# Performance work log

Hardware: AMD Instinct MI355X
Metric: run time of the kernel (lower is better)

## Reference

```python
import jax, jax.numpy as jnp
import numpy as np

N_NODES = 100000
N_EDGES = 1000000
NODE_DIM = 64
HIDDEN_DIM = 128


def setup_inputs() -> dict:
    key = jax.random.key(0)
    ks = jax.random.split(key, 9)
    x = jax.random.normal(ks[0], (N_NODES, NODE_DIM), dtype=jnp.float32)
    y = jax.random.normal(ks[1], (N_NODES, NODE_DIM), dtype=jnp.float32)
    edge_index = jax.random.randint(ks[2], (2, N_EDGES), 0, N_NODES, dtype=jnp.int64)
    pos_x = jax.random.normal(ks[3], (N_NODES, 3), dtype=jnp.float32)
    pos_y = jax.random.normal(ks[4], (N_NODES, 3), dtype=jnp.float32)
    in_dim = NODE_DIM * 2 + 1
    # Kaiming-uniform-ish init like torch Linear
    lim1 = 1.0 / np.sqrt(in_dim)
    lim2 = 1.0 / np.sqrt(HIDDEN_DIM)
    W1 = jax.random.uniform(ks[5], (in_dim, HIDDEN_DIM), jnp.float32, -lim1, lim1)
    b1 = jax.random.uniform(ks[6], (HIDDEN_DIM,), jnp.float32, -lim1, lim1)
    W2 = jax.random.uniform(ks[7], (HIDDEN_DIM, 1), jnp.float32, -lim2, lim2)
    b2 = jax.random.uniform(ks[8], (1,), jnp.float32, -lim2, lim2)
    return {"x": x, "y": y, "edge_index": edge_index, "pos_x": pos_x,
            "pos_y": pos_y, "W1": W1, "b1": b1, "W2": W2, "b2": b2}


def reference(x, y, edge_index, pos_x, pos_y, W1, b1, W2, b2):
    src = edge_index[0]
    dst = edge_index[1]
    # per-edge euclidean distance between endpoint positions  [E]
    d = pos_x[src] - pos_y[dst]                      # [E, 3]
    dist = jnp.sqrt(jnp.sum(d * d, axis=1))          # [E]
    # gather + concat: [E, node_dim*2 + 1]
    mlp_in = jnp.concatenate([x[src], y[dst], dist[:, None]], axis=1)
    h = jax.nn.relu(mlp_in @ W1 + b1)                # [E, hidden]
    out = jax.nn.relu(h @ W2 + b2)                   # [E, 1]
    return out
```

## Files before the change

kernel.cpp:

```cpp
#include <hip/hip_runtime.h>
#include <hip/hip_bf16.h>


constexpr int NDIM  = 64;
constexpr int HID   = 128;
constexpr int KPAD  = 136;

typedef __attribute__((ext_vector_type(8))) short  short8;
typedef __attribute__((ext_vector_type(4))) int    int4v;
typedef __attribute__((ext_vector_type(4))) float  floatx4;

__device__ __forceinline__ short f2bf(float f) {
    union { __hip_bfloat16 h; short s; } cv;
    cv.h = __float2bfloat16(f);
    return cv.s;
}

__device__ __forceinline__ int pack2(float a, float b) {
    union { __hip_bfloat162 h; int u; } cv;
    cv.h = __float22bfloat162_rn(float2{a, b});
    return cv.u;
}

__device__ __forceinline__ short8 make_afrag_f32(const float* rp) {
    const floatx4 f0 = *reinterpret_cast<const floatx4*>(rp);
    const floatx4 f1 = *reinterpret_cast<const floatx4*>(rp + 4);
    union { int4v i; short8 s8; } cv;
    cv.i.x = pack2(f0.x, f0.y);
    cv.i.y = pack2(f0.z, f0.w);
    cv.i.z = pack2(f1.x, f1.y);
    cv.i.w = pack2(f1.z, f1.w);
    return cv.s8;
}

__global__ __launch_bounds__(256) void cvt_kernel(
    const float* __restrict__ xin, const float* __restrict__ yin,
    short* __restrict__ xb, short* __restrict__ yb, int nfl)
{
    const int stride = gridDim.x * blockDim.x;
    const int n8 = nfl >> 3;
    for (int i = blockIdx.x * blockDim.x + threadIdx.x; i < n8; i += stride) {
        {
            const floatx4 f0 = *reinterpret_cast<const floatx4*>(xin + i * 8);
            const floatx4 f1 = *reinterpret_cast<const floatx4*>(xin + i * 8 + 4);
            union { int4v v; short8 s; } c;
            c.v.x = pack2(f0.x, f0.y); c.v.y = pack2(f0.z, f0.w);
            c.v.z = pack2(f1.x, f1.y); c.v.w = pack2(f1.z, f1.w);
            *reinterpret_cast<short8*>(xb + i * 8) = c.s;
        }
        {
            const floatx4 f0 = *reinterpret_cast<const floatx4*>(yin + i * 8);
            const floatx4 f1 = *reinterpret_cast<const floatx4*>(yin + i * 8 + 4);
            union { int4v v; short8 s; } c;
            c.v.x = pack2(f0.x, f0.y); c.v.y = pack2(f0.z, f0.w);
            c.v.z = pack2(f1.x, f1.y); c.v.w = pack2(f1.z, f1.w);
            *reinterpret_cast<short8*>(yb + i * 8) = c.s;
        }
    }
}

template <bool BF16GATHER>
__global__ __launch_bounds__(256, 4) void edge_mlp_kernel(
    const float* __restrict__ x, const float* __restrict__ y,
    const short* __restrict__ xb, const short* __restrict__ yb,
    const int*  __restrict__ ei, const float* __restrict__ px,
    const float* __restrict__ py, const float* __restrict__ W1,
    const float* __restrict__ b1, const float* __restrict__ W2,
    const float* __restrict__ b2, float* __restrict__ out, int E)
{
    __shared__ __align__(16) short Wt[HID * KPAD];

    const int tid = threadIdx.x;

    for (int base = 0; base < HID * HID; base += 256 * 8) {
        float f[8];
#pragma unroll
        for (int u = 0; u < 8; ++u) f[u] = W1[base + u * 256 + tid];
#pragma unroll
        for (int u = 0; u < 8; ++u) {
            int i = base + u * 256 + tid;
            Wt[(i & 127) * KPAD + (i >> 7)] = f2bf(f[u]);
        }
    }
    if (tid < HID) {
        const int n = tid;
        Wt[n * KPAD + 128] = f2bf(W1[128 * HID + n]);
        Wt[n * KPAD + 129] = f2bf(b1[n]);
#pragma unroll
        for (int j = 130; j < 136; ++j) Wt[n * KPAD + j] = 0;
    }
    __syncthreads();

    const int lane = tid & 63;
    const int wave = tid >> 6;
    const int quad = lane >> 4;
    const int lm   = lane & 15;

    float w2v[8];
#pragma unroll
    for (int t = 0; t < 8; ++t) w2v[t] = W2[t * 16 + lm];
    const float b2s = b2[0];

    const int* __restrict__ srcp = ei;
    const int* __restrict__ dstp = ei + E;

    const int sel5 = (quad == 0) ? 128 : 0;

    const int ntiles = (E + 127) / 128;
    for (int tile = blockIdx.x; tile < ntiles; tile += gridDim.x) {
        const int mb = tile * 128 + wave * 32;
        int m0 = mb + lm;       if (m0 >= E) m0 = E - 1;
        int m1 = mb + 16 + lm;  if (m1 >= E) m1 = E - 1;
        const int src0 = srcp[m0], dst0 = dstp[m0];
        const int src1 = srcp[m1], dst1 = dstp[m1];

        float dd = 0.f;
        if (lane < 32) {
            const int ps = (lane < 16) ? src0 : src1;
            const int pd = (lane < 16) ? dst0 : dst1;
            const float ax = px[ps * 3 + 0] - py[pd * 3 + 0];
            const float ay = px[ps * 3 + 1] - py[pd * 3 + 1];
            const float az = px[ps * 3 + 2] - py[pd * 3 + 2];
            dd = sqrtf(ax * ax + ay * ay + az * az);
        }
        const float dist0 = __shfl(dd, lm, 64);
        const float dist1 = __shfl(dd, lm + 16, 64);

        short8 fa[4], fb[4];
#pragma unroll
        for (int s = 0; s < 4; ++s) {
            const int kk = s * 32 + quad * 8;
            if (BF16GATHER) {
                const short* pa = (s < 2) ? (xb + src0 * NDIM + kk)
                                          : (yb + dst0 * NDIM + (kk - 64));
                const short* pb = (s < 2) ? (xb + src1 * NDIM + kk)
                                          : (yb + dst1 * NDIM + (kk - 64));
                fa[s] = *reinterpret_cast<const short8*>(pa);
                fb[s] = *reinterpret_cast<const short8*>(pb);
            } else {
                fa[s] = make_afrag_f32((s < 2) ? (x + src0 * NDIM + kk)
                                               : (y + dst0 * NDIM + (kk - 64)));
                fb[s] = make_afrag_f32((s < 2) ? (x + src1 * NDIM + kk)
                                               : (y + dst1 * NDIM + (kk - 64)));
            }
        }
        short8 fa4, fb4;
        {
            union { int4v i; short8 s8; } ca, cb;
            const int d0 = (quad == 0) ? pack2(dist0, 1.0f) : 0;
            const int d1 = (quad == 0) ? pack2(dist1, 1.0f) : 0;
            ca.i = int4v{d0, 0, 0, 0};
            cb.i = int4v{d1, 0, 0, 0};
            fa4 = ca.s8; fb4 = cb.s8;
        }

        float p0 = 0.f, p1 = 0.f, p2 = 0.f, p3 = 0.f;
        float q0 = 0.f, q1 = 0.f, q2 = 0.f, q3 = 0.f;

        int zoff = 0;
        asm volatile("" : "+v"(zoff));
        const short* wr  = Wt + zoff + lm * KPAD + quad * 8;
        const short* wr5 = Wt + zoff + lm * KPAD + sel5;

#pragma unroll
        for (int half = 0; half < 2; ++half) {
            if (half) __builtin_amdgcn_sched_barrier(0);

            floatx4 aA[4], aB[4];
#pragma unroll
            for (int u = 0; u < 4; ++u) {
                aA[u] = floatx4{0.f, 0.f, 0.f, 0.f};
                aB[u] = floatx4{0.f, 0.f, 0.f, 0.f};
            }
#pragma unroll
            for (int u = 0; u < 4; ++u) {
                const int t = half * 4 + u;
                const short* base = wr + t * (16 * KPAD);
                const short8 bg0 = *reinterpret_cast<const short8*>(base);
                const short8 bg1 = *reinterpret_cast<const short8*>(base + 32);
                const short8 bg2 = *reinterpret_cast<const short8*>(base + 64);
                const short8 bg3 = *reinterpret_cast<const short8*>(base + 96);
                const short8 bg4 = *reinterpret_cast<const short8*>(wr5 + t * (16 * KPAD));
                aA[u] = __builtin_amdgcn_mfma_f32_16x16x32_bf16(fa[0], bg0, aA[u], 0, 0, 0);
                aB[u] = __builtin_amdgcn_mfma_f32_16x16x32_bf16(fb[0], bg0, aB[u], 0, 0, 0);
                aA[u] = __builtin_amdgcn_mfma_f32_16x16x32_bf16(fa[1], bg1, aA[u], 0, 0, 0);
                aB[u] = __builtin_amdgcn_mfma_f32_16x16x32_bf16(fb[1], bg1, aB[u], 0, 0, 0);
                aA[u] = __builtin_amdgcn_mfma_f32_16x16x32_bf16(fa[2], bg2, aA[u], 0, 0, 0);
                aB[u] = __builtin_amdgcn_mfma_f32_16x16x32_bf16(fb[2], bg2, aB[u], 0, 0, 0);
                aA[u] = __builtin_amdgcn_mfma_f32_16x16x32_bf16(fa[3], bg3, aA[u], 0, 0, 0);
                aB[u] = __builtin_amdgcn_mfma_f32_16x16x32_bf16(fb[3], bg3, aB[u], 0, 0, 0);
                aA[u] = __builtin_amdgcn_mfma_f32_16x16x32_bf16(fa4,   bg4, aA[u], 0, 0, 0);
                aB[u] = __builtin_amdgcn_mfma_f32_16x16x32_bf16(fb4,   bg4, aB[u], 0, 0, 0);
            }
#pragma unroll
            for (int u = 0; u < 4; ++u) {
                const float w = w2v[half * 4 + u];
                p0 += fmaxf(aA[u][0], 0.f) * w;
                p1 += fmaxf(aA[u][1], 0.f) * w;
                p2 += fmaxf(aA[u][2], 0.f) * w;
                p3 += fmaxf(aA[u][3], 0.f) * w;
                q0 += fmaxf(aB[u][0], 0.f) * w;
                q1 += fmaxf(aB[u][1], 0.f) * w;
                q2 += fmaxf(aB[u][2], 0.f) * w;
                q3 += fmaxf(aB[u][3], 0.f) * w;
            }
        }

#pragma unroll
        for (int off = 1; off < 16; off <<= 1) {
            p0 += __shfl_xor(p0, off, 64);
            p1 += __shfl_xor(p1, off, 64);
            p2 += __shfl_xor(p2, off, 64);
            p3 += __shfl_xor(p3, off, 64);
            q0 += __shfl_xor(q0, off, 64);
            q1 += __shfl_xor(q1, off, 64);
            q2 += __shfl_xor(q2, off, 64);
            q3 += __shfl_xor(q3, off, 64);
        }
        if (lm < 4) {
            const float vA = (lm == 0) ? p0 : (lm == 1) ? p1 : (lm == 2) ? p2 : p3;
            const float vB = (lm == 0) ? q0 : (lm == 1) ? q1 : (lm == 2) ? q2 : q3;
            const int eA = mb + quad * 4 + lm;
            const int eB = mb + 16 + quad * 4 + lm;
            if (eA < E) out[eA] = fmaxf(vA + b2s, 0.f);
            if (eB < E) out[eB] = fmaxf(vB + b2s, 0.f);
        }
    }
}

extern "C" void kernel_launch(void* const* d_in, const int* in_sizes, int n_in,
                              void* d_out, int out_size, void* d_ws, size_t ws_size,
                              hipStream_t stream)
{
    const float* x  = (const float*)d_in[0];
    const float* y  = (const float*)d_in[1];
    const int*   ei = (const int*)  d_in[2];
    const float* px = (const float*)d_in[3];
    const float* py = (const float*)d_in[4];
    const float* W1 = (const float*)d_in[5];
    const float* b1 = (const float*)d_in[6];
    const float* W2 = (const float*)d_in[7];
    const float* b2 = (const float*)d_in[8];
    float* out = (float*)d_out;
    const int E = in_sizes[2] / 2;
    const int nnode_elems = in_sizes[0];

    const size_t need = (size_t)nnode_elems * 2 * sizeof(short);
    if (ws_size >= need) {
        short* xb = (short*)d_ws;
        short* yb = xb + nnode_elems;
        cvt_kernel<<<dim3(1024), dim3(256), 0, stream>>>(x, y, xb, yb, nnode_elems);
        edge_mlp_kernel<true><<<dim3(1024), dim3(256), 0, stream>>>(
            x, y, xb, yb, ei, px, py, W1, b1, W2, b2, out, E);
    } else {
        edge_mlp_kernel<false><<<dim3(1024), dim3(256), 0, stream>>>(
            x, y, nullptr, nullptr, ei, px, py, W1, b1, W2, b2, out, E);
    }
}
```

Baseline: 163.3 us.

## Fold dist and bias into epilogue FMAs and cache W1 fragments in registers

Drops the fifth, mostly-zero MFMA per output tile that carried the distance and bias columns. Bias now seeds the accumulators and the distance term is applied as a scalar FMA before ReLU, with both rounded to bf16 to match the old numerics. Six of the eight W1 column groups are preloaded into registers once per block, which removes most per-tile LDS reads. To make room for those registers, launch bounds drop from 4 to 2 blocks per CU, which halves the occupancy available to hide gather latency.

```diff
diff --git a/kernel.cpp b/kernel.cpp
--- a/kernel.cpp
+++ b/kernel.cpp
@@ -31,6 +31,12 @@
     cv.i.z = pack2(f1.x, f1.y);
     cv.i.w = pack2(f1.z, f1.w);
     return cv.s8;
+}
+
+__device__ __forceinline__ float bf2f(short s) {
+    union { __hip_bfloat16 h; short v; } cv;
+    cv.v = s;
+    return __bfloat162float(cv.h);
 }
 
 __global__ __launch_bounds__(256) void cvt_kernel(
@@ -60,7 +66,7 @@
 }
 
 template <bool BF16GATHER>
-__global__ __launch_bounds__(256, 4) void edge_mlp_kernel(
+__global__ __launch_bounds__(256, 2) void edge_mlp_kernel(
     const float* __restrict__ x, const float* __restrict__ y,
     const short* __restrict__ xb, const short* __restrict__ yb,
     const int*  __restrict__ ei, const float* __restrict__ px,
@@ -69,7 +75,6 @@
     const float* __restrict__ b2, float* __restrict__ out, int E)
 {
     __shared__ __align__(16) short Wt[HID * KPAD];
-
     const int tid = threadIdx.x;
 
     for (int base = 0; base < HID * HID; base += 256 * 8) {
@@ -81,13 +86,6 @@
             int i = base + u * 256 + tid;
             Wt[(i & 127) * KPAD + (i >> 7)] = f2bf(f[u]);
         }
-    }
-    if (tid < HID) {
-        const int n = tid;
-        Wt[n * KPAD + 128] = f2bf(W1[128 * HID + n]);
-        Wt[n * KPAD + 129] = f2bf(b1[n]);
-#pragma unroll
-        for (int j = 130; j < 136; ++j) Wt[n * KPAD + j] = 0;
     }
     __syncthreads();
 
@@ -96,15 +94,26 @@
     const int quad = lane >> 4;
     const int lm   = lane & 15;
 
-    float w2v[8];
-#pragma unroll
-    for (int t = 0; t < 8; ++t) w2v[t] = W2[t * 16 + lm];
+    float w2v[8], w1rv[8], b1v[8];
+#pragma unroll
+    for (int t = 0; t < 8; ++t) {
+        const int n = t * 16 + lm;
+        w2v[t]  = W2[n];
+        w1rv[t] = bf2f(f2bf(W1[128 * HID + n]));
+        b1v[t]  = bf2f(f2bf(b1[n]));
+    }
     const float b2s = b2[0];
 
     const int* __restrict__ srcp = ei;
     const int* __restrict__ dstp = ei + E;
 
-    const int sel5 = (quad == 0) ? 128 : 0;
+    const short* wr = Wt + lm * KPAD + quad * 8;
+    short8 wg[6][4];
+#pragma unroll
+    for (int t = 0; t < 6; ++t)
+#pragma unroll
+        for (int c = 0; c < 4; ++c)
+            wg[t][c] = *reinterpret_cast<const short8*>(wr + t * (16 * KPAD) + c * 32);
 
     const int ntiles = (E + 127) / 128;
     for (int tile = blockIdx.x; tile < ntiles; tile += gridDim.x) {
@@ -123,35 +132,32 @@
             const float az = px[ps * 3 + 2] - py[pd * 3 + 2];
             dd = sqrtf(ax * ax + ay * ay + az * az);
         }
-        const float dist0 = __shfl(dd, lm, 64);
-        const float dist1 = __shfl(dd, lm + 16, 64);
+        float dfA[4], dfB[4];
+#pragma unroll
+        for (int r = 0; r < 4; ++r) {
+            const float dA = __shfl(dd, quad * 4 + r, 64);
+            const float dB = __shfl(dd, 16 + quad * 4 + r, 64);
+            dfA[r] = bf2f(f2bf(dA));
+            dfB[r] = bf2f(f2bf(dB));
+        }
 
         short8 fa[4], fb[4];
 #pragma unroll
-        for (int s = 0; s < 4; ++s) {
-            const int kk = s * 32 + quad * 8;
+        for (int c = 0; c < 4; ++c) {
+            const int kk = c * 32 + quad * 8;
             if (BF16GATHER) {
-                const short* pa = (s < 2) ? (xb + src0 * NDIM + kk)
+                const short* pa = (c < 2) ? (xb + src0 * NDIM + kk)
                                           : (yb + dst0 * NDIM + (kk - 64));
-                const short* pb = (s < 2) ? (xb + src1 * NDIM + kk)
+                const short* pb = (c < 2) ? (xb + src1 * NDIM + kk)
                                           : (yb + dst1 * NDIM + (kk - 64));
-                fa[s] = *reinterpret_cast<const short8*>(pa);
-                fb[s] = *reinterpret_cast<const short8*>(pb);
+                fa[c] = *reinterpret_cast<const short8*>(pa);
+                fb[c] = *reinterpret_cast<const short8*>(pb);
             } else {
-                fa[s] = make_afrag_f32((s < 2) ? (x + src0 * NDIM + kk)
+                fa[c] = make_afrag_f32((c < 2) ? (x + src0 * NDIM + kk)
                                                : (y + dst0 * NDIM + (kk - 64)));
-                fb[s] = make_afrag_f32((s < 2) ? (x + src1 * NDIM + kk)
+                fb[c] = make_afrag_f32((c < 2) ? (x + src1 * NDIM + kk)
                                                : (y + dst1 * NDIM + (kk - 64)));
             }
-        }
-        short8 fa4, fb4;
-        {
-            union { int4v i; short8 s8; } ca, cb;
-            const int d0 = (quad == 0) ? pack2(dist0, 1.0f) : 0;
-            const int d1 = (quad == 0) ? pack2(dist1, 1.0f) : 0;
-            ca.i = int4v{d0, 0, 0, 0};
-            cb.i = int4v{d1, 0, 0, 0};
-            fa4 = ca.s8; fb4 = cb.s8;
         }
 
         float p0 = 0.f, p1 = 0.f, p2 = 0.f, p3 = 0.f;
@@ -159,8 +165,7 @@
 
         int zoff = 0;
         asm volatile("" : "+v"(zoff));
-        const short* wr  = Wt + zoff + lm * KPAD + quad * 8;
-        const short* wr5 = Wt + zoff + lm * KPAD + sel5;
+        const short* wrs = Wt + zoff + lm * KPAD + quad * 8;
 
 #pragma unroll
         for (int half = 0; half < 2; ++half) {
@@ -169,18 +174,24 @@
             floatx4 aA[4], aB[4];
 #pragma unroll
             for (int u = 0; u < 4; ++u) {
-                aA[u] = floatx4{0.f, 0.f, 0.f, 0.f};
-                aB[u] = floatx4{0.f, 0.f, 0.f, 0.f};
+                const int t = half * 4 + u;
+                const float bi = b1v[t];
+                aA[u] = floatx4{bi, bi, bi, bi};
+                aB[u] = floatx4{bi, bi, bi, bi};
             }
 #pragma unroll
             for (int u = 0; u < 4; ++u) {
                 const int t = half * 4 + u;
-                const short* base = wr + t * (16 * KPAD);
-                const short8 bg0 = *reinterpret_cast<const short8*>(base);
-                const short8 bg1 = *reinterpret_cast<const short8*>(base + 32);
-                const short8 bg2 = *reinterpret_cast<const short8*>(base + 64);
-                const short8 bg3 = *reinterpret_cast<const short8*>(base + 96);
-                const short8 bg4 = *reinterpret_cast<const short8*>(wr5 + t * (16 * KPAD));
+                short8 bg0, bg1, bg2, bg3;
+                if (t < 6) {
+                    bg0 = wg[t][0]; bg1 = wg[t][1]; bg2 = wg[t][2]; bg3 = wg[t][3];
+                } else {
+                    const short* bp = wrs + t * (16 * KPAD);
+                    bg0 = *reinterpret_cast<const short8*>(bp);
+                    bg1 = *reinterpret_cast<const short8*>(bp + 32);
+                    bg2 = *reinterpret_cast<const short8*>(bp + 64);
+                    bg3 = *reinterpret_cast<const short8*>(bp + 96);
+                }
                 aA[u] = __builtin_amdgcn_mfma_f32_16x16x32_bf16(fa[0], bg0, aA[u], 0, 0, 0);
                 aB[u] = __builtin_amdgcn_mfma_f32_16x16x32_bf16(fb[0], bg0, aB[u], 0, 0, 0);
                 aA[u] = __builtin_amdgcn_mfma_f32_16x16x32_bf16(fa[1], bg1, aA[u], 0, 0, 0);
@@ -189,20 +200,20 @@
                 aB[u] = __builtin_amdgcn_mfma_f32_16x16x32_bf16(fb[2], bg2, aB[u], 0, 0, 0);
                 aA[u] = __builtin_amdgcn_mfma_f32_16x16x32_bf16(fa[3], bg3, aA[u], 0, 0, 0);
                 aB[u] = __builtin_amdgcn_mfma_f32_16x16x32_bf16(fb[3], bg3, aB[u], 0, 0, 0);
-                aA[u] = __builtin_amdgcn_mfma_f32_16x16x32_bf16(fa4,   bg4, aA[u], 0, 0, 0);
-                aB[u] = __builtin_amdgcn_mfma_f32_16x16x32_bf16(fb4,   bg4, aB[u], 0, 0, 0);
             }
 #pragma unroll
             for (int u = 0; u < 4; ++u) {
-                const float w = w2v[half * 4 + u];
-                p0 += fmaxf(aA[u][0], 0.f) * w;
-                p1 += fmaxf(aA[u][1], 0.f) * w;
-                p2 += fmaxf(aA[u][2], 0.f) * w;
-                p3 += fmaxf(aA[u][3], 0.f) * w;
-                q0 += fmaxf(aB[u][0], 0.f) * w;
-                q1 += fmaxf(aB[u][1], 0.f) * w;
-                q2 += fmaxf(aB[u][2], 0.f) * w;
-                q3 += fmaxf(aB[u][3], 0.f) * w;
+                const int t = half * 4 + u;
+                const float w  = w2v[t];
+                const float wr1 = w1rv[t];
+                p0 += fmaxf(fmaf(dfA[0], wr1, aA[u][0]), 0.f) * w;
+                p1 += fmaxf(fmaf(dfA[1], wr1, aA[u][1]), 0.f) * w;
+                p2 += fmaxf(fmaf(dfA[2], wr1, aA[u][2]), 0.f) * w;
+                p3 += fmaxf(fmaf(dfA[3], wr1, aA[u][3]), 0.f) * w;
+                q0 += fmaxf(fmaf(dfB[0], wr1, aB[u][0]), 0.f) * w;
+                q1 += fmaxf(fmaf(dfB[1], wr1, aB[u][1]), 0.f) * w;
+                q2 += fmaxf(fmaf(dfB[2], wr1, aB[u][2]), 0.f) * w;
+                q3 += fmaxf(fmaf(dfB[3], wr1, aB[u][3]), 0.f) * w;
             }
         }
 
```

Result: no change. 166.3 us (+1.8%).
